# Optimization experiments

Hardware: AMD Instinct MI355X
Metric: run time of the kernel (lower is better)

## Reference

```python
import jax, jax.numpy as jnp
import numpy as np

N, DIN, D, HID, E, OUT = 16384, 1024, 1024, 256, 10, 1024


def setup_inputs() -> dict:
    key = jax.random.key(0)
    ks = jax.random.split(key, 13)
    g = lambda k, sh, s=0.02: (jax.random.normal(k, sh, jnp.float32) * s)
    return {
        "x": jax.random.normal(ks[0], (N, DIN), jnp.float32),
        "top_k": 2,
        # input projection (input_dim -> adjusted_dim)
        "Wp": g(ks[1], (DIN, D)), "bp": jnp.zeros((D,), jnp.float32),
        # MHA with seq_len=1 reduces exactly to out_proj(v_proj(x))
        "Wv": g(ks[2], (D, D)), "bv": jnp.zeros((D,), jnp.float32),
        "Wo": g(ks[3], (D, D)), "bo": jnp.zeros((D,), jnp.float32),
        # gate
        "Wg": g(ks[4], (D, E)), "bg": jnp.zeros((E,), jnp.float32),
        # experts: Linear(D,256) -> ReLU -> Linear(256,OUT), stacked over E
        "W1": g(ks[5], (E, D, HID)), "b1": jnp.zeros((E, HID), jnp.float32),
        "W2": g(ks[6], (E, HID, OUT)), "b2": jnp.zeros((E, OUT), jnp.float32),
    }


def reference(x, top_k, Wp, bp, Wv, bv, Wo, bo, Wg, bg, W1, b1, W2, b2):
    n = x.shape[0]
    e = Wg.shape[1]
    h = x @ Wp + bp                               # [N, D] input projection
    # MultiheadAttention with seq_len=1: softmax over one key == 1 exactly,
    # so attn output == out_proj(v_proj(h)).
    a = (h @ Wv + bv) @ Wo + bo                   # [N, D]
    gate_probs = jax.nn.softmax(a @ Wg + bg, axis=-1)   # [N, E]
    vals, idx = jax.lax.top_k(gate_probs, top_k)        # [N, K]
    vals = vals / jnp.sum(vals, axis=-1, keepdims=True)
    # scatter normalized top-k probs into dense combine weights [N, E]
    combine = jnp.zeros((n, e), a.dtype).at[jnp.arange(n)[:, None], idx].set(vals)
    # dense all-expert MLP, masked by combine weights (zeros kill unrouted experts)
    hid = jax.nn.relu(jnp.einsum("nd,edh->enh", a, W1) + b1[:, None, :])  # [E, N, HID]
    hid = hid * combine.T[:, :, None]                                      # weight tokens
    out = jnp.einsum("enh,eho->no", hid, W2) + combine @ b2                # [N, OUT]
    return out
```

## Files before the change

kernel.cpp:

```cpp
#include <hip/hip_runtime.h>
#include <hip/hip_bf16.h>
#include <math.h>

#define N_TOK   16384
#define D_IN    1024
#define D_MODEL 1024
#define HID     256
#define NEXP    10
#define D_OUT   1024

#define EPAD 128
#define A_CAP (2*N_TOK + NEXP*EPAD)

typedef __attribute__((ext_vector_type(8))) __bf16 bf16x8;
typedef __attribute__((ext_vector_type(4))) float floatx4;

__device__ __forceinline__ int xcd_chunk(int orig, int nwg)
{
    const int q = nwg >> 3, r = nwg & 7;
    const int c = orig & 7, j = orig >> 3;
    return (c < r ? c * (q + 1) : r * (q + 1) + (c - r) * q) + j;
}

__device__ __forceinline__ bf16x8 lds_frag(const short* base, int row, int chunk)
{
    return *(const bf16x8*)(base + row * 64 + (chunk << 3));
}

__device__ __forceinline__ void tile_plain(const short* As, const short* Bs,
                                           int wm, int wn, int lane, floatx4 acc[4][4])
{
    const int m15 = lane & 15, quad = lane >> 4, sw = m15 & 7;
#pragma unroll
    for (int kk = 0; kk < 2; ++kk) {
        bf16x8 af[4], bfr[4];
#pragma unroll
        for (int i = 0; i < 4; ++i)
            af[i] = lds_frag(As, wm * 64 + i * 16 + m15, ((kk << 2) + quad) ^ sw);
#pragma unroll
        for (int j = 0; j < 4; ++j)
            bfr[j] = lds_frag(Bs, wn * 64 + j * 16 + m15, ((kk << 2) + quad) ^ sw);
#pragma unroll
        for (int i = 0; i < 4; ++i)
#pragma unroll
            for (int j = 0; j < 4; ++j)
                acc[i][j] = __builtin_amdgcn_mfma_f32_16x16x32_bf16(af[i], bfr[j],
                                                                    acc[i][j], 0, 0, 0);
    }
}

__device__ __forceinline__ void tile_split(const short* As, const short* Bs,
                                           int wm, int wn, int lane, floatx4 acc[4][4])
{
    const int m15 = lane & 15, quad = lane >> 4, sw = m15 & 7;
    bf16x8 ah[4], al[4], bh[4], bl[4];
#pragma unroll
    for (int i = 0; i < 4; ++i) {
        int r = wm * 64 + i * 16 + m15;
        ah[i] = lds_frag(As, r, quad ^ sw);
        al[i] = lds_frag(As, r, (4 + quad) ^ sw);
    }
#pragma unroll
    for (int j = 0; j < 4; ++j) {
        int r = wn * 64 + j * 16 + m15;
        bh[j] = lds_frag(Bs, r, quad ^ sw);
        bl[j] = lds_frag(Bs, r, (4 + quad) ^ sw);
    }
#pragma unroll
    for (int i = 0; i < 4; ++i)
#pragma unroll
        for (int j = 0; j < 4; ++j) {
            floatx4 c = acc[i][j];
            c = __builtin_amdgcn_mfma_f32_16x16x32_bf16(ah[i], bh[j], c, 0, 0, 0);
            c = __builtin_amdgcn_mfma_f32_16x16x32_bf16(ah[i], bl[j], c, 0, 0, 0);
            c = __builtin_amdgcn_mfma_f32_16x16x32_bf16(al[i], bh[j], c, 0, 0, 0);
            acc[i][j] = c;
        }
}

__device__ __forceinline__ void tile_split_a64(const short* As, const short* Bs,
                                               int wm, int wn, int lane,
                                               floatx4 acc[2][4])
{
    const int m15 = lane & 15, quad = lane >> 4, sw = m15 & 7;
    bf16x8 ah[2], al[2], bh[4];
#pragma unroll
    for (int i = 0; i < 2; ++i) {
        int r = wm * 32 + i * 16 + m15;
        ah[i] = lds_frag(As, r, quad ^ sw);
        al[i] = lds_frag(As, r, (4 + quad) ^ sw);
    }
#pragma unroll
    for (int j = 0; j < 4; ++j) {
        int r = wn * 64 + j * 16 + m15;
        bh[j] = lds_frag(Bs, r, quad ^ sw);
    }
#pragma unroll
    for (int i = 0; i < 2; ++i)
#pragma unroll
        for (int j = 0; j < 4; ++j) {
            floatx4 c = acc[i][j];
            c = __builtin_amdgcn_mfma_f32_16x16x32_bf16(ah[i], bh[j], c, 0, 0, 0);
            c = __builtin_amdgcn_mfma_f32_16x16x32_bf16(al[i], bh[j], c, 0, 0, 0);
            acc[i][j] = c;
        }
}

__global__ __launch_bounds__(256)
void gemm_split_kernel(const __hip_bfloat16* Ahi_, const __hip_bfloat16* Alo_,
                       const __hip_bfloat16* Bhi_, const __hip_bfloat16* Blo_,
                       const float* __restrict__ bias,
                       __hip_bfloat16* Chi_, __hip_bfloat16* Clo_, int K, int N,
                       size_t zsA, size_t zsB, size_t zsC)
{
    __shared__ __align__(16) short As[128 * 64];
    __shared__ __align__(16) short Bs[128 * 64];
    const short* Ahi = (const short*)Ahi_;
    const short* Alo = (const short*)Alo_;
    const short* Bhi = (const short*)Bhi_;
    const short* Blo = (const short*)Blo_;

    const int tid = threadIdx.x, lane = tid & 63, w = tid >> 6;
    const int wm = w & 1, wn = w >> 1;
    const size_t zA = (size_t)blockIdx.z * zsA;
    const size_t zB = (size_t)blockIdx.z * zsB;
    const size_t zC = (size_t)blockIdx.z * zsC;
    const int lin = blockIdx.y * gridDim.x + blockIdx.x;
    const int lgc = xcd_chunk(lin, gridDim.x * gridDim.y);
    const int row0 = (lgc / gridDim.x) * 128, col0 = (lgc % gridDim.x) * 128;
    const int lr = lane >> 3;
    const int g = (lane & 7) ^ lr;
    const int plane = g >> 2, colel = (g & 3) * 8;

    const short* pA[4];
    const short* pB[4];
#pragma unroll
    for (int i = 0; i < 4; ++i) {
        int r = w * 32 + i * 8 + lr;
        pA[i] = (plane ? Alo : Ahi) + zA + (size_t)(row0 + r) * K + colel;
        pB[i] = (plane ? Blo : Bhi) + zB + (size_t)(col0 + r) * K + colel;
    }

    floatx4 acc[4][4];
#pragma unroll
    for (int i = 0; i < 4; ++i)
#pragma unroll
        for (int j = 0; j < 4; ++j) acc[i][j] = (floatx4)(0.f);

    bf16x8 va[4], vb[4];
#pragma unroll
    for (int i = 0; i < 4; ++i) {
        va[i] = *(const bf16x8*)(pA[i]);
        vb[i] = *(const bf16x8*)(pB[i]);
    }

    for (int k0 = 0; k0 < K; k0 += 32) {
        __syncthreads();
#pragma unroll
        for (int i = 0; i < 4; ++i) {
            *(bf16x8*)(&As[(w * 32 + i * 8) * 64 + lane * 8]) = va[i];
            *(bf16x8*)(&Bs[(w * 32 + i * 8) * 64 + lane * 8]) = vb[i];
        }
        __syncthreads();
        if (k0 + 32 < K) {
#pragma unroll
            for (int i = 0; i < 4; ++i) {
                va[i] = *(const bf16x8*)(pA[i] + k0 + 32);
                vb[i] = *(const bf16x8*)(pB[i] + k0 + 32);
            }
        }
        tile_split(As, Bs, wm, wn, lane, acc);
    }

    const int m15 = lane & 15, quad = lane >> 4;
#pragma unroll
    for (int i = 0; i < 4; ++i) {
#pragma unroll
        for (int t = 0; t < 4; ++t) {
            int row = row0 + wm * 64 + i * 16 + quad * 4 + t;
            size_t rb = zC + (size_t)row * N;
#pragma unroll
            for (int j = 0; j < 4; ++j) {
                int col = col0 + wn * 64 + j * 16 + m15;
                float v = acc[i][j][t] + bias[col];
                __hip_bfloat16 hi = __float2bfloat16(v);
                Chi_[rb + col] = hi;
                if (Clo_) Clo_[rb + col] = __float2bfloat16(v - __bfloat162float(hi));
            }
        }
    }
}

__global__ __launch_bounds__(256)
void expert1_kernel(const __hip_bfloat16* x_hi_, const __hip_bfloat16* x_lo_,
                    const __hip_bfloat16* W1e_hi_,
                    const float* __restrict__ b1eff,
                    const int* __restrict__ assign_token, const int* __restrict__ offs,
                    const __hip_bfloat16* zrow_, __hip_bfloat16* hid_)
{
    __shared__ __align__(16) short As[64 * 64];
    __shared__ __align__(16) short Bs[128 * 64];
    const short* Xhi = (const short*)x_hi_;
    const short* Xlo = (const short*)x_lo_;
    const short* zrow = (const short*)zrow_;

    const int tid = threadIdx.x, lane = tid & 63, w = tid >> 6;
    const int wm = w & 1, wn = w >> 1;
    const int lin = blockIdx.y * gridDim.x + blockIdx.x;
    const int lgc = xcd_chunk(lin, gridDim.x * gridDim.y);
    const int row0 = (lgc / gridDim.x) * 64, col0 = (lgc % gridDim.x) * 128;
    const int lr = lane >> 3;
    const int g = (lane & 7) ^ lr;
    const int plane = g >> 2, colel = (g & 3) * 8;

    int e = NEXP - 1;
    for (int q = 0; q < NEXP; ++q) { if (row0 < offs[q + 1]) { e = q; break; } }
    const short* Bh = (const short*)W1e_hi_ + (size_t)e * HID * D_IN;

    const short* pA[2];
    const short* pB[4];
#pragma unroll
    for (int i = 0; i < 2; ++i) {
        int r = w * 16 + i * 8 + lr;
        int tok = assign_token[row0 + r];
        pA[i] = (tok >= 0 ? (plane ? Xlo : Xhi) + (size_t)tok * D_IN : zrow) + colel;
    }
#pragma unroll
    for (int i = 0; i < 4; ++i) {
        int r = w * 32 + i * 8 + lr;
        pB[i] = Bh + (size_t)(col0 + r) * D_IN + colel;
    }

    floatx4 acc[2][4];
#pragma unroll
    for (int i = 0; i < 2; ++i)
#pragma unroll
        for (int j = 0; j < 4; ++j) acc[i][j] = (floatx4)(0.f);

    bf16x8 va[2], vb[4];
#pragma unroll
    for (int i = 0; i < 2; ++i) va[i] = *(const bf16x8*)(pA[i]);
#pragma unroll
    for (int i = 0; i < 4; ++i) vb[i] = *(const bf16x8*)(pB[i]);

    for (int k0 = 0; k0 < D_IN; k0 += 32) {
        __syncthreads();
#pragma unroll
        for (int i = 0; i < 2; ++i)
            *(bf16x8*)(&As[(w * 16 + i * 8) * 64 + lane * 8]) = va[i];
#pragma unroll
        for (int i = 0; i < 4; ++i)
            *(bf16x8*)(&Bs[(w * 32 + i * 8) * 64 + lane * 8]) = vb[i];
        __syncthreads();
        if (k0 + 32 < D_IN) {
#pragma unroll
            for (int i = 0; i < 2; ++i) va[i] = *(const bf16x8*)(pA[i] + k0 + 32);
#pragma unroll
            for (int i = 0; i < 4; ++i) vb[i] = *(const bf16x8*)(pB[i] + k0 + 32);
        }
        tile_split_a64(As, Bs, wm, wn, lane, acc);
    }

    const int m15 = lane & 15, quad = lane >> 4;
#pragma unroll
    for (int i = 0; i < 2; ++i) {
#pragma unroll
        for (int t = 0; t < 4; ++t) {
            int row = row0 + wm * 32 + i * 16 + quad * 4 + t;
            size_t rb = (size_t)row * HID;
#pragma unroll
            for (int j = 0; j < 4; ++j) {
                int col = col0 + wn * 64 + j * 16 + m15;
                float v = acc[i][j][t] + b1eff[(size_t)e * HID + col];
                hid_[rb + col] = __float2bfloat16(fmaxf(v, 0.f));
            }
        }
    }
}

__global__ __launch_bounds__(256)
void expert2_kernel(const __hip_bfloat16* hid_, const __hip_bfloat16* W2t_,
                    const int* __restrict__ offs, __hip_bfloat16* exp_out_)
{
    __shared__ __align__(16) short As[128 * 64];
    __shared__ __align__(16) short Bs[128 * 64];
    const short* A = (const short*)hid_;

    const int tid = threadIdx.x, lane = tid & 63, w = tid >> 6;
    const int wm = w & 1, wn = w >> 1;
    const int lin = blockIdx.y * gridDim.x + blockIdx.x;
    const int lgc = xcd_chunk(lin, gridDim.x * gridDim.y);
    const int row0 = (lgc / gridDim.x) * 128, col0 = (lgc % gridDim.x) * 128;
    const int lr = lane >> 3, g = (lane & 7) ^ lr, colel = g * 8;

    int e = NEXP - 1;
    for (int q = 0; q < NEXP; ++q) { if (row0 < offs[q + 1]) { e = q; break; } }
    const short* B = (const short*)W2t_ + (size_t)e * D_OUT * HID;

    const short* pA[4];
    const short* pB[4];
#pragma unroll
    for (int i = 0; i < 4; ++i) {
        int r = w * 32 + i * 8 + lr;
        pA[i] = A + (size_t)(row0 + r) * HID + colel;
        pB[i] = B + (size_t)(col0 + r) * HID + colel;
    }

    floatx4 acc[4][4];
#pragma unroll
    for (int i = 0; i < 4; ++i)
#pragma unroll
        for (int j = 0; j < 4; ++j) acc[i][j] = (floatx4)(0.f);

    bf16x8 va[4], vb[4];
#pragma unroll
    for (int i = 0; i < 4; ++i) {
        va[i] = *(const bf16x8*)(pA[i]);
        vb[i] = *(const bf16x8*)(pB[i]);
    }

    for (int k0 = 0; k0 < HID; k0 += 64) {
        __syncthreads();
#pragma unroll
        for (int i = 0; i < 4; ++i) {
            *(bf16x8*)(&As[(w * 32 + i * 8) * 64 + lane * 8]) = va[i];
            *(bf16x8*)(&Bs[(w * 32 + i * 8) * 64 + lane * 8]) = vb[i];
        }
        __syncthreads();
        if (k0 + 64 < HID) {
#pragma unroll
            for (int i = 0; i < 4; ++i) {
                va[i] = *(const bf16x8*)(pA[i] + k0 + 64);
                vb[i] = *(const bf16x8*)(pB[i] + k0 + 64);
            }
        }
        tile_plain(As, Bs, wm, wn, lane, acc);
    }

    const int m15 = lane & 15, quad = lane >> 4;
#pragma unroll
    for (int i = 0; i < 4; ++i) {
#pragma unroll
        for (int t = 0; t < 4; ++t) {
            int row = row0 + wm * 64 + i * 16 + quad * 4 + t;
            size_t rb = (size_t)row * D_OUT;
#pragma unroll
            for (int j = 0; j < 4; ++j) {
                int col = col0 + wn * 64 + j * 16 + m15;
                exp_out_[rb + col] = __float2bfloat16(acc[i][j][t]);
            }
        }
    }
}

__global__ __launch_bounds__(256)
void convert_gate_kernel(const float* __restrict__ x, const float* __restrict__ MgT,
                         const float* __restrict__ bgeff,
                         __hip_bfloat16* __restrict__ x_hi, __hip_bfloat16* __restrict__ x_lo,
                         int* __restrict__ route_e, float* __restrict__ route_w)
{
    const int wave = threadIdx.x >> 6, lane = threadIdx.x & 63;
    const int n = blockIdx.x * 4 + wave;
    const float* xrow = x + (size_t)n * D_IN;

    float4 v[4];
#pragma unroll
    for (int it = 0; it < 4; ++it)
        v[it] = *(const float4*)(xrow + it * 256 + lane * 4);

    float p[NEXP];
#pragma unroll
    for (int e = 0; e < NEXP; ++e) p[e] = 0.f;

#pragma unroll
    for (int it = 0; it < 4; ++it) {
        const int d = it * 256 + lane * 4;
        union { __hip_bfloat16 b[4]; short4 s; } uh, ul;
        uh.b[0] = __float2bfloat16(v[it].x); ul.b[0] = __float2bfloat16(v[it].x - __bfloat162float(uh.b[0]));
        uh.b[1] = __float2bfloat16(v[it].y); ul.b[1] = __float2bfloat16(v[it].y - __bfloat162float(uh.b[1]));
        uh.b[2] = __float2bfloat16(v[it].z); ul.b[2] = __float2bfloat16(v[it].z - __bfloat162float(uh.b[2]));
        uh.b[3] = __float2bfloat16(v[it].w); ul.b[3] = __float2bfloat16(v[it].w - __bfloat162float(uh.b[3]));
        *(short4*)(x_hi + (size_t)n * D_IN + d) = uh.s;
        *(short4*)(x_lo + (size_t)n * D_IN + d) = ul.s;
#pragma unroll
        for (int e = 0; e < NEXP; ++e) {
            const float4 m = *(const float4*)(MgT + (size_t)e * 1024 + d);
            p[e] += v[it].x * m.x + v[it].y * m.y + v[it].z * m.z + v[it].w * m.w;
        }
    }

#pragma unroll
    for (int e = 0; e < NEXP; ++e) {
        float t = p[e];
        for (int off = 32; off > 0; off >>= 1) t += __shfl_down(t, off);
        p[e] = t;
    }
    if (lane == 0) {
        float lg[NEXP];
#pragma unroll
        for (int e = 0; e < NEXP; ++e) lg[e] = p[e] + bgeff[e];
        int e0 = 0; float v0 = lg[0];
        for (int e = 1; e < NEXP; ++e) if (lg[e] > v0) { v0 = lg[e]; e0 = e; }
        int e1 = -1; float v1 = -3.0e38f;
        for (int e = 0; e < NEXP; ++e) {
            if (e == e0) continue;
            if (lg[e] > v1) { v1 = lg[e]; e1 = e; }
        }
        float w0 = 1.f / (1.f + expf(v1 - v0));
        float w1 = 1.f - w0;
        route_e[n * 2]     = e0;
        route_e[n * 2 + 1] = e1;
        route_w[n * 2]     = w0;
        route_w[n * 2 + 1] = w1;
    }
}

__global__ __launch_bounds__(256)
void count_kernel(const int* __restrict__ route_e, int* __restrict__ counts)
{
    __shared__ int h[NEXP];
    if (threadIdx.x < NEXP) h[threadIdx.x] = 0;
    __syncthreads();
    const int i = blockIdx.x * 512 + threadIdx.x;
    atomicAdd(&h[route_e[i]], 1);
    atomicAdd(&h[route_e[i + 256]], 1);
    __syncthreads();
    if (threadIdx.x < NEXP) atomicAdd(&counts[threadIdx.x], h[threadIdx.x]);
}

__global__ __launch_bounds__(256)
void transpose_cvt_kernel(const float* __restrict__ in, __hip_bfloat16* out_hi,
                          __hip_bfloat16* out_lo, int R, int C)
{
    __shared__ float t[32][33];
    const size_t zoff = (size_t)blockIdx.z * R * C;
    in += zoff; out_hi += zoff; if (out_lo) out_lo += zoff;
    const int c0 = blockIdx.x * 32, r0 = blockIdx.y * 32;
    const int tx = threadIdx.x & 31, ty = threadIdx.x >> 5;
#pragma unroll
    for (int i = 0; i < 4; ++i)
        t[ty + i * 8][tx] = in[(size_t)(r0 + ty + i * 8) * C + (c0 + tx)];
    __syncthreads();
#pragma unroll
    for (int i = 0; i < 4; ++i) {
        float v = t[tx][ty + i * 8];
        size_t o = (size_t)(c0 + ty + i * 8) * R + (r0 + tx);
        __hip_bfloat16 hi = __float2bfloat16(v);
        out_hi[o] = hi;
        if (out_lo) out_lo[o] = __float2bfloat16(v - __bfloat162float(hi));
    }
}

__global__ __launch_bounds__(256)
void convert_plain_kernel(const float* __restrict__ in,
                          __hip_bfloat16* __restrict__ out_hi,
                          __hip_bfloat16* __restrict__ out_lo)
{
    const int i = blockIdx.x * 256 + threadIdx.x;
    const float4 v = ((const float4*)in)[i];
    union { __hip_bfloat16 b[4]; short4 s; } uh, ul;
    uh.b[0] = __float2bfloat16(v.x); ul.b[0] = __float2bfloat16(v.x - __bfloat162float(uh.b[0]));
    uh.b[1] = __float2bfloat16(v.y); ul.b[1] = __float2bfloat16(v.y - __bfloat162float(uh.b[1]));
    uh.b[2] = __float2bfloat16(v.z); ul.b[2] = __float2bfloat16(v.z - __bfloat162float(uh.b[2]));
    uh.b[3] = __float2bfloat16(v.w); ul.b[3] = __float2bfloat16(v.w - __bfloat162float(uh.b[3]));
    ((short4*)out_hi)[i] = uh.s;
    ((short4*)out_lo)[i] = ul.s;
}

__global__ __launch_bounds__(256)
void bias2_kernel(const float* __restrict__ bp, const float* __restrict__ bv,
                  const float* __restrict__ bo,
                  const __hip_bfloat16* __restrict__ Pt_hi,
                  const __hip_bfloat16* __restrict__ Pt_lo,
                  const __hip_bfloat16* __restrict__ Wot_hi,
                  const __hip_bfloat16* __restrict__ Wot_lo,
                  float* __restrict__ beff2)
{
    const int wave = threadIdx.x >> 6, lane = threadIdx.x & 63;
    const int n = blockIdx.x * 4 + wave;
    float acc = 0.f;
    for (int k = lane; k < D_MODEL; k += 64) {
        const size_t o = (size_t)n * D_MODEL + k;
        float pt = __bfloat162float(Pt_hi[o]) + __bfloat162float(Pt_lo[o]);
        float wo = __bfloat162float(Wot_hi[o]) + __bfloat162float(Wot_lo[o]);
        acc += bp[k] * pt + bv[k] * wo;
    }
    for (int off = 32; off > 0; off >>= 1) acc += __shfl_down(acc, off);
    if (lane == 0) beff2[n] = acc + bo[n];
}

__global__ __launch_bounds__(256)
void b1eff_kernel(const float* __restrict__ beff2,
                  const __hip_bfloat16* __restrict__ W1t_hi,
                  const __hip_bfloat16* __restrict__ W1t_lo,
                  const float* __restrict__ b1, float* __restrict__ b1eff)
{
    const int wave = threadIdx.x >> 6, lane = threadIdx.x & 63;
    const int n = blockIdx.x * 4 + wave;
    const size_t base = (size_t)n * D_MODEL;
    float acc = 0.f;
    for (int k = lane; k < D_MODEL; k += 64)
        acc += beff2[k] * (__bfloat162float(W1t_hi[base + k]) +
                           __bfloat162float(W1t_lo[base + k]));
    for (int off = 32; off > 0; off >>= 1) acc += __shfl_down(acc, off);
    if (lane == 0) b1eff[n] = acc + b1[n];
}

__global__ __launch_bounds__(256)
void wchain_kernel(const float* __restrict__ A, const float* __restrict__ B,
                   float* __restrict__ Cm, int trans)
{
    const int wave = threadIdx.x >> 6, lane = threadIdx.x & 63;
    const int m = blockIdx.x * 4 + wave;
    float acc[NEXP];
#pragma unroll
    for (int e = 0; e < NEXP; ++e) acc[e] = 0.f;
    const float* ar = A + (size_t)m * 1024;
    for (int d = lane; d < 1024; d += 64) {
        float av = ar[d];
        const float* br = B + (size_t)d * NEXP;
#pragma unroll
        for (int e = 0; e < NEXP; ++e) acc[e] += av * br[e];
    }
#pragma unroll
    for (int e = 0; e < NEXP; ++e) {
        float v = acc[e];
        for (int off = 32; off > 0; off >>= 1) v += __shfl_down(v, off);
        if (lane == 0) Cm[trans ? ((size_t)e * 1024 + m) : ((size_t)m * NEXP + e)] = v;
    }
}

__global__ __launch_bounds__(256)
void bias_eff_kernel(const float* __restrict__ bp, const float* __restrict__ bv,
                     const float* __restrict__ bo, const float* __restrict__ bg,
                     const float* __restrict__ Wg, const float* __restrict__ t1,
                     const float* __restrict__ t2, float* __restrict__ bgeff)
{
    __shared__ float red[256];
    const int tid = threadIdx.x;
    float acc[NEXP];
#pragma unroll
    for (int e = 0; e < NEXP; ++e) acc[e] = 0.f;
    for (int d = tid; d < 1024; d += 256) {
        float o = bo[d], v = bv[d], p = bp[d];
#pragma unroll
        for (int e = 0; e < NEXP; ++e)
            acc[e] += o * Wg[d * NEXP + e] + v * t1[d * NEXP + e] + p * t2[d * NEXP + e];
    }
    for (int e = 0; e < NEXP; ++e) {
        red[tid] = acc[e];
        __syncthreads();
        for (int s = 128; s > 0; s >>= 1) {
            if (tid < s) red[tid] += red[tid + s];
            __syncthreads();
        }
        if (tid == 0) bgeff[e] = red[0] + bg[e];
        __syncthreads();
    }
}

__global__ __launch_bounds__(256)
void init_kernel(int* __restrict__ counts, int* __restrict__ cursors,
                 int* __restrict__ assign_token, int* __restrict__ zrow_i,
                 float* __restrict__ fzero)
{
    int i = blockIdx.x * 256 + threadIdx.x;
    if (i < NEXP) { counts[i] = 0; cursors[i] = 0; }
    if (i < 512) zrow_i[i] = 0;
    if (i < 1024) fzero[i] = 0.f;
    if (i < A_CAP) assign_token[i] = -1;
}

__global__ void offsets_kernel(const int* __restrict__ counts, int* __restrict__ offs)
{
    if (threadIdx.x == 0 && blockIdx.x == 0) {
        int acc = 0;
        for (int e = 0; e < NEXP; ++e) {
            offs[e] = acc;
            acc += (counts[e] + EPAD - 1) / EPAD * EPAD;
        }
        offs[NEXP] = acc;
    }
}

__global__ __launch_bounds__(256)
void scatter_kernel(const int* __restrict__ route_e,
                    const int* __restrict__ offs, int* __restrict__ cursors,
                    int* __restrict__ assign_token, int* __restrict__ slot_of)
{
    const int i = blockIdx.x * 256 + threadIdx.x;
    const int lane = threadIdx.x & 63;
    const int e = route_e[i];
    int slot = 0;
#pragma unroll
    for (int q = 0; q < NEXP; ++q) {
        unsigned long long mask = __ballot(e == q);
        if (e == q) {
            const int leader = (int)__ffsll((long long)mask) - 1;
            const int rank = (int)__popcll(mask & ((1ull << lane) - 1ull));
            int base = 0;
            if (lane == leader) base = atomicAdd(&cursors[q], (int)__popcll(mask));
            base = __shfl(base, leader);
            slot = offs[q] + base + rank;
        }
    }
    assign_token[slot] = i >> 1;
    slot_of[i] = slot;
}

__global__ __launch_bounds__(256)
void combine_kernel(const __hip_bfloat16* __restrict__ exp_out,
                    const int* __restrict__ slot_of, const int* __restrict__ route_e,
                    const float* __restrict__ route_w, const float* __restrict__ b2,
                    float* __restrict__ out)
{
    const int n = blockIdx.x;
    const int c = threadIdx.x * 4;
    const int s0 = slot_of[n * 2],  s1 = slot_of[n * 2 + 1];
    const int e0 = route_e[n * 2],  e1 = route_e[n * 2 + 1];
    const float w0 = route_w[n * 2], w1 = route_w[n * 2 + 1];

    union U { float2 f2; __hip_bfloat16 b[4]; } u0, u1;
    u0.f2 = *(const float2*)(exp_out + (size_t)s0 * D_OUT + c);
    u1.f2 = *(const float2*)(exp_out + (size_t)s1 * D_OUT + c);
    const float4 bb0 = *(const float4*)(b2 + (size_t)e0 * D_OUT + c);
    const float4 bb1 = *(const float4*)(b2 + (size_t)e1 * D_OUT + c);

    float4 o;
    o.x = w0 * (__bfloat162float(u0.b[0]) + bb0.x) + w1 * (__bfloat162float(u1.b[0]) + bb1.x);
    o.y = w0 * (__bfloat162float(u0.b[1]) + bb0.y) + w1 * (__bfloat162float(u1.b[1]) + bb1.y);
    o.z = w0 * (__bfloat162float(u0.b[2]) + bb0.z) + w1 * (__bfloat162float(u1.b[2]) + bb1.z);
    o.w = w0 * (__bfloat162float(u0.b[3]) + bb0.w) + w1 * (__bfloat162float(u1.b[3]) + bb1.w);
    *(float4*)(out + (size_t)n * D_OUT + c) = o;
}

extern "C" void kernel_launch(void* const* d_in, const int* in_sizes, int n_in,
                              void* d_out, int out_size, void* d_ws, size_t ws_size,
                              hipStream_t stream)
{
    const float* x  = (const float*)d_in[0];
    const float* Wp = (const float*)d_in[2];
    const float* bp = (const float*)d_in[3];
    const float* Wv = (const float*)d_in[4];
    const float* bv = (const float*)d_in[5];
    const float* Wo = (const float*)d_in[6];
    const float* bo = (const float*)d_in[7];
    const float* Wg = (const float*)d_in[8];
    const float* bg = (const float*)d_in[9];
    const float* W1 = (const float*)d_in[10];
    const float* b1 = (const float*)d_in[11];
    const float* W2 = (const float*)d_in[12];
    const float* b2 = (const float*)d_in[13];
    float* out = (float*)d_out;

    char* W = (char*)d_ws;
    typedef __hip_bfloat16 bf;
    bf* x_hi  = (bf*)(W + 0);
    bf* x_lo  = (bf*)(W + 33554432);
    bf* exp_out = (bf*)(W + 0);
    bf* hid   = (bf*)(W + 69730304);
    bf* Wvr_hi = (bf*)(W + 88080384);
    bf* Wvr_lo = (bf*)(W + 90177536);
    bf* Wpr_hi = (bf*)(W + 92274688);
    bf* Wpr_lo = (bf*)(W + 94371840);
    float* fzero = (float*)(W + 96468992);
    float* beff2 = (float*)(W + 96473088);
    bf* W1t_lo   = (bf*)(W + 100663296);
    bf* W1eff_hi = (bf*)(W + 105906176);
    float* b1eff = (float*)(W + 116391936);
    bf* Pt_hi  = (bf*)(W + 134217728);
    bf* Pt_lo  = (bf*)(W + 136314880);
    bf* Mrow_hi = (bf*)(W + 138412032);
    bf* Mrow_lo = (bf*)(W + 140509184);
    bf* Wot_hi = (bf*)(W + 142606336);
    bf* Wot_lo = (bf*)(W + 144703488);
    bf* W1t    = (bf*)(W + 146800640);
    bf* W2t    = (bf*)(W + 152043520);
    bf*    zrow         = (bf*)(W + 157286400);
    int*   route_e      = (int*)(W + 157288448);
    float* route_w      = (float*)(W + 157419520);
    int*   slot_of      = (int*)(W + 157550592);
    int*   assign_token = (int*)(W + 157681664);
    int*   counts       = (int*)(W + 157817856);
    int*   offs         = (int*)(W + 157817920);
    int*   cursors      = (int*)(W + 157817984);
    float* MgT          = (float*)(W + 157818048);
    float* t1           = (float*)(W + 157859008);
    float* t2           = (float*)(W + 157899968);
    float* bgeff        = (float*)(W + 157940928);

    dim3 blk(256);

    init_kernel<<<(A_CAP + 255) / 256, blk, 0, stream>>>(counts, cursors, assign_token,
                                                         (int*)zrow, fzero);

    transpose_cvt_kernel<<<dim3(32, 32, 1), blk, 0, stream>>>(Wo, Wot_hi, Wot_lo, D_MODEL, D_MODEL);
    convert_plain_kernel<<<1024, blk, 0, stream>>>(Wv, Wvr_hi, Wvr_lo);
    convert_plain_kernel<<<1024, blk, 0, stream>>>(Wp, Wpr_hi, Wpr_lo);
    transpose_cvt_kernel<<<dim3(HID / 32, D_MODEL / 32, NEXP), blk, 0, stream>>>(W1, W1t, W1t_lo, D_MODEL, HID);
    transpose_cvt_kernel<<<dim3(D_OUT / 32, HID / 32, NEXP), blk, 0, stream>>>(W2, W2t, nullptr, HID, D_OUT);

    wchain_kernel<<<256, blk, 0, stream>>>(Wo, Wg, t1, 0);
    wchain_kernel<<<256, blk, 0, stream>>>(Wv, t1, t2, 0);
    wchain_kernel<<<256, blk, 0, stream>>>(Wp, t2, MgT, 1);
    bias_eff_kernel<<<1, blk, 0, stream>>>(bp, bv, bo, bg, Wg, t1, t2, bgeff);

    dim3 pgrid(D_MODEL / 128, D_MODEL / 128, 1);
    gemm_split_kernel<<<pgrid, blk, 0, stream>>>(Wot_hi, Wot_lo, Wvr_hi, Wvr_lo, fzero,
                                                 Pt_hi, Pt_lo, D_MODEL, D_MODEL, 0, 0, 0);
    gemm_split_kernel<<<pgrid, blk, 0, stream>>>(Wpr_hi, Wpr_lo, Pt_hi, Pt_lo, fzero,
                                                 Mrow_hi, Mrow_lo, D_MODEL, D_MODEL, 0, 0, 0);
    bias2_kernel<<<D_MODEL / 4, blk, 0, stream>>>(bp, bv, bo, Pt_hi, Pt_lo,
                                                  Wot_hi, Wot_lo, beff2);
    b1eff_kernel<<<NEXP * HID / 4, blk, 0, stream>>>(beff2, W1t, W1t_lo, b1, b1eff);
    dim3 wgrid(D_IN / 128, HID / 128, NEXP);
    gemm_split_kernel<<<wgrid, blk, 0, stream>>>(W1t, W1t_lo, Mrow_hi, Mrow_lo, fzero,
                                                 W1eff_hi, nullptr, D_MODEL, D_IN,
                                                 (size_t)HID * D_MODEL, 0,
                                                 (size_t)HID * D_IN);

    convert_gate_kernel<<<N_TOK / 4, blk, 0, stream>>>(x, MgT, bgeff, x_hi, x_lo,
                                                       route_e, route_w);
    count_kernel<<<2 * N_TOK / 512, blk, 0, stream>>>(route_e, counts);
    offsets_kernel<<<1, 64, 0, stream>>>(counts, offs);
    scatter_kernel<<<2 * N_TOK / 256, blk, 0, stream>>>(route_e, offs, cursors,
                                                        assign_token, slot_of);

    expert1_kernel<<<dim3(HID / 128, A_CAP / 64), blk, 0, stream>>>(
        x_hi, x_lo, W1eff_hi, b1eff, assign_token, offs, zrow, hid);
    expert2_kernel<<<dim3(D_OUT / 128, A_CAP / 128), blk, 0, stream>>>(
        hid, W2t, offs, exp_out);
    combine_kernel<<<N_TOK, blk, 0, stream>>>(exp_out, slot_of, route_e, route_w, b2, out);
}
```

Measured before the change: 520.8 us.

## Fuse expert MLP layers with on-the-fly x split and merge prep conversions

Replaces the two expert GEMM kernels with one fused kernel: each 64-row block computes the full 256-wide hidden layer into LDS, then loops over the output columns against W2, so the hidden activations never go through global memory. The fused kernel reads x as fp32 and splits it into hi/lo bf16 in registers, so the gate kernel no longer writes x_hi/x_lo copies. The five weight transpose/convert launches are merged into one prep kernel. In exchange, each block now holds far more LDS and its 64-row tile only gives a grid of about 530 blocks, which lowers occupancy and parallelism, and the x conversion is repeated inside the GEMM loop.

```diff
diff --git a/kernel.cpp b/kernel.cpp
--- a/kernel.cpp
+++ b/kernel.cpp
@@ -73,34 +73,6 @@
             floatx4 c = acc[i][j];
             c = __builtin_amdgcn_mfma_f32_16x16x32_bf16(ah[i], bh[j], c, 0, 0, 0);
             c = __builtin_amdgcn_mfma_f32_16x16x32_bf16(ah[i], bl[j], c, 0, 0, 0);
-            c = __builtin_amdgcn_mfma_f32_16x16x32_bf16(al[i], bh[j], c, 0, 0, 0);
-            acc[i][j] = c;
-        }
-}
-
-__device__ __forceinline__ void tile_split_a64(const short* As, const short* Bs,
-                                               int wm, int wn, int lane,
-                                               floatx4 acc[2][4])
-{
-    const int m15 = lane & 15, quad = lane >> 4, sw = m15 & 7;
-    bf16x8 ah[2], al[2], bh[4];
-#pragma unroll
-    for (int i = 0; i < 2; ++i) {
-        int r = wm * 32 + i * 16 + m15;
-        ah[i] = lds_frag(As, r, quad ^ sw);
-        al[i] = lds_frag(As, r, (4 + quad) ^ sw);
-    }
-#pragma unroll
-    for (int j = 0; j < 4; ++j) {
-        int r = wn * 64 + j * 16 + m15;
-        bh[j] = lds_frag(Bs, r, quad ^ sw);
-    }
-#pragma unroll
-    for (int i = 0; i < 2; ++i)
-#pragma unroll
-        for (int j = 0; j < 4; ++j) {
-            floatx4 c = acc[i][j];
-            c = __builtin_amdgcn_mfma_f32_16x16x32_bf16(ah[i], bh[j], c, 0, 0, 0);
             c = __builtin_amdgcn_mfma_f32_16x16x32_bf16(al[i], bh[j], c, 0, 0, 0);
             acc[i][j] = c;
         }
@@ -192,172 +164,198 @@
 }
 
 __global__ __launch_bounds__(256)
-void expert1_kernel(const __hip_bfloat16* x_hi_, const __hip_bfloat16* x_lo_,
-                    const __hip_bfloat16* W1e_hi_,
-                    const float* __restrict__ b1eff,
-                    const int* __restrict__ assign_token, const int* __restrict__ offs,
-                    const __hip_bfloat16* zrow_, __hip_bfloat16* hid_)
+void expert_fused_kernel(const float* __restrict__ x, const float* __restrict__ fzero,
+                         const __hip_bfloat16* W1e_hi_, const float* __restrict__ b1eff,
+                         const __hip_bfloat16* W2t_,
+                         const int* __restrict__ assign_token, const int* __restrict__ offs,
+                         __hip_bfloat16* exp_out_)
 {
     __shared__ __align__(16) short As[64 * 64];
-    __shared__ __align__(16) short Bs[128 * 64];
-    const short* Xhi = (const short*)x_hi_;
-    const short* Xlo = (const short*)x_lo_;
-    const short* zrow = (const short*)zrow_;
+    __shared__ __align__(16) short Bs[2][128 * 64];
+    __shared__ __align__(16) short Hs[4][64 * 64];
 
     const int tid = threadIdx.x, lane = tid & 63, w = tid >> 6;
-    const int wm = w & 1, wn = w >> 1;
-    const int lin = blockIdx.y * gridDim.x + blockIdx.x;
-    const int lgc = xcd_chunk(lin, gridDim.x * gridDim.y);
-    const int row0 = (lgc / gridDim.x) * 64, col0 = (lgc % gridDim.x) * 128;
+    const int lgc = xcd_chunk(blockIdx.x, gridDim.x);
+    const int row0 = lgc * 64;
     const int lr = lane >> 3;
     const int g = (lane & 7) ^ lr;
-    const int plane = g >> 2, colel = (g & 3) * 8;
+    const int plane = g >> 2, kofs = (g & 3) * 8;
+    const int m15 = lane & 15, quad = lane >> 4, sw = m15 & 7;
 
     int e = NEXP - 1;
     for (int q = 0; q < NEXP; ++q) { if (row0 < offs[q + 1]) { e = q; break; } }
     const short* Bh = (const short*)W1e_hi_ + (size_t)e * HID * D_IN;
-
-    const short* pA[2];
-    const short* pB[4];
+    const short* W2 = (const short*)W2t_ + (size_t)e * D_OUT * HID;
+
+    const float* pX[2];
 #pragma unroll
     for (int i = 0; i < 2; ++i) {
         int r = w * 16 + i * 8 + lr;
         int tok = assign_token[row0 + r];
-        pA[i] = (tok >= 0 ? (plane ? Xlo : Xhi) + (size_t)tok * D_IN : zrow) + colel;
-    }
-#pragma unroll
-    for (int i = 0; i < 4; ++i) {
-        int r = w * 32 + i * 8 + lr;
-        pB[i] = Bh + (size_t)(col0 + r) * D_IN + colel;
-    }
-
-    floatx4 acc[2][4];
-#pragma unroll
-    for (int i = 0; i < 2; ++i)
-#pragma unroll
-        for (int j = 0; j < 4; ++j) acc[i][j] = (floatx4)(0.f);
-
-    bf16x8 va[2], vb[4];
-#pragma unroll
-    for (int i = 0; i < 2; ++i) va[i] = *(const bf16x8*)(pA[i]);
-#pragma unroll
-    for (int i = 0; i < 4; ++i) vb[i] = *(const bf16x8*)(pB[i]);
+        pX[i] = (tok >= 0 ? x + (size_t)tok * D_IN : fzero) + kofs;
+    }
+    const short* pB[8];
+#pragma unroll
+    for (int i = 0; i < 8; ++i) {
+        int r = w * 32 + (i & 3) * 8 + lr + (i >= 4 ? 128 : 0);
+        pB[i] = Bh + (size_t)r * D_IN + kofs;
+    }
+
+    floatx4 acc1[4][4];
+#pragma unroll
+    for (int i = 0; i < 4; ++i)
+#pragma unroll
+        for (int j = 0; j < 4; ++j) acc1[i][j] = (floatx4)(0.f);
+
+    float4 fa[2][2];
+    bf16x8 vb[8];
+#pragma unroll
+    for (int i = 0; i < 2; ++i) {
+        fa[i][0] = *(const float4*)(pX[i]);
+        fa[i][1] = *(const float4*)(pX[i] + 4);
+    }
+#pragma unroll
+    for (int i = 0; i < 8; ++i) vb[i] = *(const bf16x8*)(pB[i]);
 
     for (int k0 = 0; k0 < D_IN; k0 += 32) {
         __syncthreads();
 #pragma unroll
-        for (int i = 0; i < 2; ++i)
-            *(bf16x8*)(&As[(w * 16 + i * 8) * 64 + lane * 8]) = va[i];
-#pragma unroll
-        for (int i = 0; i < 4; ++i)
-            *(bf16x8*)(&Bs[(w * 32 + i * 8) * 64 + lane * 8]) = vb[i];
+        for (int i = 0; i < 2; ++i) {
+            float f[8] = { fa[i][0].x, fa[i][0].y, fa[i][0].z, fa[i][0].w,
+                           fa[i][1].x, fa[i][1].y, fa[i][1].z, fa[i][1].w };
+            union { bf16x8 v; __hip_bfloat16 h[8]; } u;
+#pragma unroll
+            for (int q2 = 0; q2 < 8; ++q2) {
+                __hip_bfloat16 h = __float2bfloat16(f[q2]);
+                u.h[q2] = plane ? __float2bfloat16(f[q2] - __bfloat162float(h)) : h;
+            }
+            *(bf16x8*)(&As[(w * 16 + i * 8) * 64 + lane * 8]) = u.v;
+        }
+#pragma unroll
+        for (int i = 0; i < 8; ++i)
+            *(bf16x8*)(&Bs[i >> 2][(w * 32 + (i & 3) * 8) * 64 + lane * 8]) = vb[i];
         __syncthreads();
         if (k0 + 32 < D_IN) {
 #pragma unroll
-            for (int i = 0; i < 2; ++i) va[i] = *(const bf16x8*)(pA[i] + k0 + 32);
-#pragma unroll
-            for (int i = 0; i < 4; ++i) vb[i] = *(const bf16x8*)(pB[i] + k0 + 32);
-        }
-        tile_split_a64(As, Bs, wm, wn, lane, acc);
-    }
-
-    const int m15 = lane & 15, quad = lane >> 4;
-#pragma unroll
-    for (int i = 0; i < 2; ++i) {
-#pragma unroll
-        for (int t = 0; t < 4; ++t) {
-            int row = row0 + wm * 32 + i * 16 + quad * 4 + t;
-            size_t rb = (size_t)row * HID;
-#pragma unroll
-            for (int j = 0; j < 4; ++j) {
-                int col = col0 + wn * 64 + j * 16 + m15;
-                float v = acc[i][j][t] + b1eff[(size_t)e * HID + col];
-                hid_[rb + col] = __float2bfloat16(fmaxf(v, 0.f));
+            for (int i = 0; i < 2; ++i) {
+                fa[i][0] = *(const float4*)(pX[i] + k0 + 32);
+                fa[i][1] = *(const float4*)(pX[i] + k0 + 36);
             }
-        }
-    }
-}
-
-__global__ __launch_bounds__(256)
-void expert2_kernel(const __hip_bfloat16* hid_, const __hip_bfloat16* W2t_,
-                    const int* __restrict__ offs, __hip_bfloat16* exp_out_)
-{
-    __shared__ __align__(16) short As[128 * 64];
-    __shared__ __align__(16) short Bs[128 * 64];
-    const short* A = (const short*)hid_;
-
-    const int tid = threadIdx.x, lane = tid & 63, w = tid >> 6;
-    const int wm = w & 1, wn = w >> 1;
-    const int lin = blockIdx.y * gridDim.x + blockIdx.x;
-    const int lgc = xcd_chunk(lin, gridDim.x * gridDim.y);
-    const int row0 = (lgc / gridDim.x) * 128, col0 = (lgc % gridDim.x) * 128;
-    const int lr = lane >> 3, g = (lane & 7) ^ lr, colel = g * 8;
-
-    int e = NEXP - 1;
-    for (int q = 0; q < NEXP; ++q) { if (row0 < offs[q + 1]) { e = q; break; } }
-    const short* B = (const short*)W2t_ + (size_t)e * D_OUT * HID;
-
-    const short* pA[4];
-    const short* pB[4];
+#pragma unroll
+            for (int i = 0; i < 8; ++i) vb[i] = *(const bf16x8*)(pB[i] + k0 + 32);
+        }
+        {
+            const short* BsT = Bs[w >> 1];
+            const int brow0 = (w & 1) * 64;
+            bf16x8 ah[4], al[4], bh[4];
+#pragma unroll
+            for (int i = 0; i < 4; ++i) {
+                int r = i * 16 + m15;
+                ah[i] = lds_frag(As, r, quad ^ sw);
+                al[i] = lds_frag(As, r, (4 + quad) ^ sw);
+            }
+#pragma unroll
+            for (int j = 0; j < 4; ++j)
+                bh[j] = lds_frag(BsT, brow0 + j * 16 + m15, quad ^ sw);
+#pragma unroll
+            for (int i = 0; i < 4; ++i)
+#pragma unroll
+                for (int j = 0; j < 4; ++j) {
+                    floatx4 c = acc1[i][j];
+                    c = __builtin_amdgcn_mfma_f32_16x16x32_bf16(ah[i], bh[j], c, 0, 0, 0);
+                    c = __builtin_amdgcn_mfma_f32_16x16x32_bf16(al[i], bh[j], c, 0, 0, 0);
+                    acc1[i][j] = c;
+                }
+        }
+    }
+
 #pragma unroll
     for (int i = 0; i < 4; ++i) {
-        int r = w * 32 + i * 8 + lr;
-        pA[i] = A + (size_t)(row0 + r) * HID + colel;
-        pB[i] = B + (size_t)(col0 + r) * HID + colel;
-    }
-
-    floatx4 acc[4][4];
+#pragma unroll
+        for (int j = 0; j < 4; ++j) {
+#pragma unroll
+            for (int t = 0; t < 4; ++t) {
+                int row = i * 16 + quad * 4 + t;
+                int col = w * 64 + j * 16 + m15;
+                float v = acc1[i][j][t] + b1eff[(size_t)e * HID + col];
+                v = fmaxf(v, 0.f);
+                __hip_bfloat16 hb = __float2bfloat16(v);
+                int kin = col & 63;
+                int pos = (kin >> 3) ^ (row & 7);
+                Hs[w][row * 64 + pos * 8 + (kin & 7)] = *(short*)&hb;
+            }
+        }
+    }
+    __syncthreads();
+
+    const int wm2 = w & 1, wn2 = w >> 1;
+    short* Bs2 = Bs[0];
+    const int g2 = (lane & 7) ^ lr, kofs2 = g2 * 8;
+    floatx4 acc2[2][4];
+    bf16x8 vb2[4];
 #pragma unroll
     for (int i = 0; i < 4; ++i)
-#pragma unroll
-        for (int j = 0; j < 4; ++j) acc[i][j] = (floatx4)(0.f);
-
-    bf16x8 va[4], vb[4];
-#pragma unroll
-    for (int i = 0; i < 4; ++i) {
-        va[i] = *(const bf16x8*)(pA[i]);
-        vb[i] = *(const bf16x8*)(pB[i]);
-    }
-
-    for (int k0 = 0; k0 < HID; k0 += 64) {
+        vb2[i] = *(const bf16x8*)(W2 + (size_t)(w * 32 + i * 8 + lr) * HID + kofs2);
+
+    for (int it = 0; it < 32; ++it) {
+        const int c0 = (it >> 2) * 128, ks = it & 3;
         __syncthreads();
 #pragma unroll
-        for (int i = 0; i < 4; ++i) {
-            *(bf16x8*)(&As[(w * 32 + i * 8) * 64 + lane * 8]) = va[i];
-            *(bf16x8*)(&Bs[(w * 32 + i * 8) * 64 + lane * 8]) = vb[i];
-        }
+        for (int i = 0; i < 4; ++i)
+            *(bf16x8*)(&Bs2[(w * 32 + i * 8) * 64 + lane * 8]) = vb2[i];
         __syncthreads();
-        if (k0 + 64 < HID) {
-#pragma unroll
-            for (int i = 0; i < 4; ++i) {
-                va[i] = *(const bf16x8*)(pA[i] + k0 + 64);
-                vb[i] = *(const bf16x8*)(pB[i] + k0 + 64);
+        if (it + 1 < 32) {
+            const int nc0 = ((it + 1) >> 2) * 128, nks = (it + 1) & 3;
+#pragma unroll
+            for (int i = 0; i < 4; ++i)
+                vb2[i] = *(const bf16x8*)(W2 + (size_t)(nc0 + w * 32 + i * 8 + lr) * HID
+                                          + nks * 64 + kofs2);
+        }
+        if (ks == 0) {
+#pragma unroll
+            for (int i = 0; i < 2; ++i)
+#pragma unroll
+                for (int j = 0; j < 4; ++j) acc2[i][j] = (floatx4)(0.f);
+        }
+        const short* Ht = Hs[ks];
+#pragma unroll
+        for (int kk = 0; kk < 2; ++kk) {
+            bf16x8 af[2], bfr[4];
+#pragma unroll
+            for (int i = 0; i < 2; ++i)
+                af[i] = lds_frag(Ht, wm2 * 32 + i * 16 + m15, ((kk << 2) + quad) ^ sw);
+#pragma unroll
+            for (int j = 0; j < 4; ++j)
+                bfr[j] = lds_frag(Bs2, wn2 * 64 + j * 16 + m15, ((kk << 2) + quad) ^ sw);
+#pragma unroll
+            for (int i = 0; i < 2; ++i)
+#pragma unroll
+                for (int j = 0; j < 4; ++j)
+                    acc2[i][j] = __builtin_amdgcn_mfma_f32_16x16x32_bf16(af[i], bfr[j],
+                                                                         acc2[i][j], 0, 0, 0);
+        }
+        if (ks == 3) {
+#pragma unroll
+            for (int i = 0; i < 2; ++i) {
+#pragma unroll
+                for (int t = 0; t < 4; ++t) {
+                    int row = row0 + wm2 * 32 + i * 16 + quad * 4 + t;
+                    size_t rb = (size_t)row * D_OUT;
+#pragma unroll
+                    for (int j = 0; j < 4; ++j) {
+                        int col = c0 + wn2 * 64 + j * 16 + m15;
+                        exp_out_[rb + col] = __float2bfloat16(acc2[i][j][t]);
+                    }
+                }
             }
         }
-        tile_plain(As, Bs, wm, wn, lane, acc);
-    }
-
-    const int m15 = lane & 15, quad = lane >> 4;
-#pragma unroll
-    for (int i = 0; i < 4; ++i) {
-#pragma unroll
-        for (int t = 0; t < 4; ++t) {
-            int row = row0 + wm * 64 + i * 16 + quad * 4 + t;
-            size_t rb = (size_t)row * D_OUT;
-#pragma unroll
-            for (int j = 0; j < 4; ++j) {
-                int col = col0 + wn * 64 + j * 16 + m15;
-                exp_out_[rb + col] = __float2bfloat16(acc[i][j][t]);
-            }
-        }
-    }
-}
-
-__global__ __launch_bounds__(256)
-void convert_gate_kernel(const float* __restrict__ x, const float* __restrict__ MgT,
-                         const float* __restrict__ bgeff,
-                         __hip_bfloat16* __restrict__ x_hi, __hip_bfloat16* __restrict__ x_lo,
-                         int* __restrict__ route_e, float* __restrict__ route_w)
+    }
+}
+
+__global__ __launch_bounds__(256)
+void gate_kernel(const float* __restrict__ x, const float* __restrict__ MgT,
+                 const float* __restrict__ bgeff,
+                 int* __restrict__ route_e, float* __restrict__ route_w)
 {
     const int wave = threadIdx.x >> 6, lane = threadIdx.x & 63;
     const int n = blockIdx.x * 4 + wave;
@@ -375,13 +373,6 @@
 #pragma unroll
     for (int it = 0; it < 4; ++it) {
         const int d = it * 256 + lane * 4;
-        union { __hip_bfloat16 b[4]; short4 s; } uh, ul;
-        uh.b[0] = __float2bfloat16(v[it].x); ul.b[0] = __float2bfloat16(v[it].x - __bfloat162float(uh.b[0]));
-        uh.b[1] = __float2bfloat16(v[it].y); ul.b[1] = __float2bfloat16(v[it].y - __bfloat162float(uh.b[1]));
-        uh.b[2] = __float2bfloat16(v[it].z); ul.b[2] = __float2bfloat16(v[it].z - __bfloat162float(uh.b[2]));
-        uh.b[3] = __float2bfloat16(v[it].w); ul.b[3] = __float2bfloat16(v[it].w - __bfloat162float(uh.b[3]));
-        *(short4*)(x_hi + (size_t)n * D_IN + d) = uh.s;
-        *(short4*)(x_lo + (size_t)n * D_IN + d) = ul.s;
 #pragma unroll
         for (int e = 0; e < NEXP; ++e) {
             const float4 m = *(const float4*)(MgT + (size_t)e * 1024 + d);
@@ -428,15 +419,16 @@
     if (threadIdx.x < NEXP) atomicAdd(&counts[threadIdx.x], h[threadIdx.x]);
 }
 
-__global__ __launch_bounds__(256)
-void transpose_cvt_kernel(const float* __restrict__ in, __hip_bfloat16* out_hi,
-                          __hip_bfloat16* out_lo, int R, int C)
-{
-    __shared__ float t[32][33];
-    const size_t zoff = (size_t)blockIdx.z * R * C;
+__device__ __forceinline__ void transpose_body(float (*t)[33], const float* in,
+                                               __hip_bfloat16* out_hi,
+                                               __hip_bfloat16* out_lo,
+                                               int R, int C, int bx, int by, int bz,
+                                               int tid)
+{
+    const size_t zoff = (size_t)bz * R * C;
     in += zoff; out_hi += zoff; if (out_lo) out_lo += zoff;
-    const int c0 = blockIdx.x * 32, r0 = blockIdx.y * 32;
-    const int tx = threadIdx.x & 31, ty = threadIdx.x >> 5;
+    const int c0 = bx * 32, r0 = by * 32;
+    const int tx = tid & 31, ty = tid >> 5;
 #pragma unroll
     for (int i = 0; i < 4; ++i)
         t[ty + i * 8][tx] = in[(size_t)(r0 + ty + i * 8) * C + (c0 + tx)];
@@ -451,20 +443,45 @@
     }
 }
 
-__global__ __launch_bounds__(256)
-void convert_plain_kernel(const float* __restrict__ in,
-                          __hip_bfloat16* __restrict__ out_hi,
-                          __hip_bfloat16* __restrict__ out_lo)
-{
-    const int i = blockIdx.x * 256 + threadIdx.x;
+__device__ __forceinline__ void plain_body(const float* in, __hip_bfloat16* oh,
+                                           __hip_bfloat16* ol, int b, int tid)
+{
+    const int i = b * 256 + tid;
     const float4 v = ((const float4*)in)[i];
-    union { __hip_bfloat16 b[4]; short4 s; } uh, ul;
-    uh.b[0] = __float2bfloat16(v.x); ul.b[0] = __float2bfloat16(v.x - __bfloat162float(uh.b[0]));
-    uh.b[1] = __float2bfloat16(v.y); ul.b[1] = __float2bfloat16(v.y - __bfloat162float(uh.b[1]));
-    uh.b[2] = __float2bfloat16(v.z); ul.b[2] = __float2bfloat16(v.z - __bfloat162float(uh.b[2]));
-    uh.b[3] = __float2bfloat16(v.w); ul.b[3] = __float2bfloat16(v.w - __bfloat162float(uh.b[3]));
-    ((short4*)out_hi)[i] = uh.s;
-    ((short4*)out_lo)[i] = ul.s;
+    union { __hip_bfloat16 bb[4]; short4 s; } uh, ul;
+    uh.bb[0] = __float2bfloat16(v.x); ul.bb[0] = __float2bfloat16(v.x - __bfloat162float(uh.bb[0]));
+    uh.bb[1] = __float2bfloat16(v.y); ul.bb[1] = __float2bfloat16(v.y - __bfloat162float(uh.bb[1]));
+    uh.bb[2] = __float2bfloat16(v.z); ul.bb[2] = __float2bfloat16(v.z - __bfloat162float(uh.bb[2]));
+    uh.bb[3] = __float2bfloat16(v.w); ul.bb[3] = __float2bfloat16(v.w - __bfloat162float(uh.bb[3]));
+    ((short4*)oh)[i] = uh.s;
+    ((short4*)ol)[i] = ul.s;
+}
+
+__global__ __launch_bounds__(256)
+void prep_convert_kernel(const float* __restrict__ Wo, const float* __restrict__ Wv,
+                         const float* __restrict__ Wp, const float* __restrict__ W1,
+                         const float* __restrict__ W2,
+                         __hip_bfloat16* Wot_hi, __hip_bfloat16* Wot_lo,
+                         __hip_bfloat16* Wvr_hi, __hip_bfloat16* Wvr_lo,
+                         __hip_bfloat16* Wpr_hi, __hip_bfloat16* Wpr_lo,
+                         __hip_bfloat16* W1t, __hip_bfloat16* W1t_lo,
+                         __hip_bfloat16* W2t)
+{
+    __shared__ float t[32][33];
+    const int b = blockIdx.x, tid = threadIdx.x;
+    if (b < 1024) {
+        transpose_body(t, Wo, Wot_hi, Wot_lo, 1024, 1024, b % 32, b / 32, 0, tid);
+    } else if (b < 3584) {
+        int c = b - 1024;
+        transpose_body(t, W1, W1t, W1t_lo, 1024, 256, c % 8, (c / 8) % 32, c / 256, tid);
+    } else if (b < 6144) {
+        int c = b - 3584;
+        transpose_body(t, W2, W2t, nullptr, 256, 1024, c % 32, (c / 32) % 8, c / 256, tid);
+    } else if (b < 7168) {
+        plain_body(Wv, Wvr_hi, Wvr_lo, b - 6144, tid);
+    } else {
+        plain_body(Wp, Wpr_hi, Wpr_lo, b - 7168, tid);
+    }
 }
 
 __global__ __launch_bounds__(256)
@@ -561,12 +578,10 @@
 
 __global__ __launch_bounds__(256)
 void init_kernel(int* __restrict__ counts, int* __restrict__ cursors,
-                 int* __restrict__ assign_token, int* __restrict__ zrow_i,
-                 float* __restrict__ fzero)
+                 int* __restrict__ assign_token, float* __restrict__ fzero)
 {
     int i = blockIdx.x * 256 + threadIdx.x;
     if (i < NEXP) { counts[i] = 0; cursors[i] = 0; }
-    if (i < 512) zrow_i[i] = 0;
     if (i < 1024) fzero[i] = 0.f;
     if (i < A_CAP) assign_token[i] = -1;
 }
@@ -655,10 +670,7 @@
 
     char* W = (char*)d_ws;
     typedef __hip_bfloat16 bf;
-    bf* x_hi  = (bf*)(W + 0);
-    bf* x_lo  = (bf*)(W + 33554432);
     bf* exp_out = (bf*)(W + 0);
-    bf* hid   = (bf*)(W + 69730304);
     bf* Wvr_hi = (bf*)(W + 88080384);
     bf* Wvr_lo = (bf*)(W + 90177536);
     bf* Wpr_hi = (bf*)(W + 92274688);
@@ -676,7 +688,6 @@
     bf* Wot_lo = (bf*)(W + 144703488);
     bf* W1t    = (bf*)(W + 146800640);
     bf* W2t    = (bf*)(W + 152043520);
-    bf*    zrow         = (bf*)(W + 157286400);
     int*   route_e      = (int*)(W + 157288448);
     float* route_w      = (float*)(W + 157419520);
     int*   slot_of      = (int*)(W + 157550592);
@@ -692,13 +703,11 @@
     dim3 blk(256);
 
     init_kernel<<<(A_CAP + 255) / 256, blk, 0, stream>>>(counts, cursors, assign_token,
-                                                         (int*)zrow, fzero);
-
-    transpose_cvt_kernel<<<dim3(32, 32, 1), blk, 0, stream>>>(Wo, Wot_hi, Wot_lo, D_MODEL, D_MODEL);
-    convert_plain_kernel<<<1024, blk, 0, stream>>>(Wv, Wvr_hi, Wvr_lo);
-    convert_plain_kernel<<<1024, blk, 0, stream>>>(Wp, Wpr_hi, Wpr_lo);
-    transpose_cvt_kernel<<<dim3(HID / 32, D_MODEL / 32, NEXP), blk, 0, stream>>>(W1, W1t, W1t_lo, D_MODEL, HID);
-    transpose_cvt_kernel<<<dim3(D_OUT / 32, HID / 32, NEXP), blk, 0, stream>>>(W2, W2t, nullptr, HID, D_OUT);
+                                                         fzero);
+
+    prep_convert_kernel<<<8192, blk, 0, stream>>>(Wo, Wv, Wp, W1, W2,
+                                                  Wot_hi, Wot_lo, Wvr_hi, Wvr_lo,
+                                                  Wpr_hi, Wpr_lo, W1t, W1t_lo, W2t);
 
     wchain_kernel<<<256, blk, 0, stream>>>(Wo, Wg, t1, 0);
     wchain_kernel<<<256, blk, 0, stream>>>(Wv, t1, t2, 0);
@@ -719,16 +728,13 @@
                                                  (size_t)HID * D_MODEL, 0,
                                                  (size_t)HID * D_IN);
 
-    convert_gate_kernel<<<N_TOK / 4, blk, 0, stream>>>(x, MgT, bgeff, x_hi, x_lo,
-                                                       route_e, route_w);
+    gate_kernel<<<N_TOK / 4, blk, 0, stream>>>(x, MgT, bgeff, route_e, route_w);
     count_kernel<<<2 * N_TOK / 512, blk, 0, stream>>>(route_e, counts);
     offsets_kernel<<<1, 64, 0, stream>>>(counts, offs);
     scatter_kernel<<<2 * N_TOK / 256, blk, 0, stream>>>(route_e, offs, cursors,
                                                         assign_token, slot_of);
 
-    expert1_kernel<<<dim3(HID / 128, A_CAP / 64), blk, 0, stream>>>(
-        x_hi, x_lo, W1eff_hi, b1eff, assign_token, offs, zrow, hid);
-    expert2_kernel<<<dim3(D_OUT / 128, A_CAP / 128), blk, 0, stream>>>(
-        hid, W2t, offs, exp_out);
+    expert_fused_kernel<<<A_CAP / 64, blk, 0, stream>>>(x, fzero, W1eff_hi, b1eff, W2t,
+                                                        assign_token, offs, exp_out);
     combine_kernel<<<N_TOK, blk, 0, stream>>>(exp_out, slot_of, route_e, route_w, b2, out);
 }
```

After: 546.6 us. 4.9% more time.
